# Optimization experiments

Measured on AMD Instinct MI355X. Metric: run time of the kernel, lower is better.

## Reference

```python
import jax, jax.numpy as jnp
import numpy as np

BATCH, SEQ_L, H, N = 16, 2048, 512, 64
DT_MIN, DT_MAX = 1e-3, 1e-1


def setup_inputs() -> dict:
    key = jax.random.key(0)
    ks = jax.random.split(key, 6)
    u = jax.random.normal(ks[0], (BATCH, SEQ_L, H), dtype=jnp.float32)
    # S4D diagonal init: stable real part, linearly spaced imaginary frequencies
    Lambda_real = -0.5 * jnp.ones((N,), dtype=jnp.float32)
    Lambda_imag = jnp.pi * jnp.arange(N, dtype=jnp.float32)
    B_real = jax.random.normal(ks[1], (H, N), dtype=jnp.float32) * (N ** -0.5)
    B_imag = jnp.zeros((H, N), dtype=jnp.float32)
    C_real = jax.random.normal(ks[2], (H, N), dtype=jnp.float32) * 0.5
    C_imag = jax.random.normal(ks[3], (H, N), dtype=jnp.float32) * 0.5
    log_dt = (jax.random.uniform(ks[4], (H,), dtype=jnp.float32)
              * (np.float32(np.log(DT_MAX)) - np.float32(np.log(DT_MIN)))
              + np.float32(np.log(DT_MIN)))
    D = jax.random.normal(ks[5], (H,), dtype=jnp.float32) * 0.01
    return {"u": u, "Lambda_real": Lambda_real, "Lambda_imag": Lambda_imag,
            "B_real": B_real, "B_imag": B_imag, "C_real": C_real,
            "C_imag": C_imag, "log_dt": log_dt, "D": D}


def reference(u, Lambda_real, Lambda_imag, B_real, B_imag, C_real, C_imag, log_dt, D):
    # u: (B, L, H)
    Lseq = u.shape[1]
    Lam = Lambda_real + 1j * Lambda_imag            # (N,)
    Bc = B_real + 1j * B_imag                        # (H, N)
    Cc = C_real + 1j * C_imag                        # (H, N)
    dt = jnp.exp(log_dt)                             # (H,)

    # ZOH discretization (matches step(): Ab = exp(dt*Lam), Bb = B*(Ab-1)/(Lam+eps))
    dtA = dt[:, None] * Lam[None, :]                 # (H, N)
    Ab = jnp.exp(dtA)
    Bb = Bc * (Ab - 1.0) / (Lam[None, :] + 1e-8)

    # Vandermonde over all channels at once: V[h,n,l] = exp(dt_h * Lam_n * l)
    ell = jnp.arange(Lseq, dtype=jnp.float32)
    V = jnp.exp(dtA[:, :, None] * ell[None, None, :])  # (H, N, L) complex
    K = jnp.einsum('hn,hnl->hl', Cc * Bb, V).real       # (H, L) real kernel

    # Causal FFT convolution along time
    x = jnp.swapaxes(u, -1, -2)                      # (B, H, L)
    nfft = 2 * Lseq
    Xf = jnp.fft.rfft(x, n=nfft)                     # (B, H, nfft/2+1)
    Kf = jnp.fft.rfft(K, n=nfft)                     # (H, nfft/2+1)
    y = jnp.fft.irfft(Xf * Kf[None], n=nfft)[..., :Lseq]

    y = y + x * D[None, :, None]                     # skip connection
    return jnp.swapaxes(y, -1, -2)                   # (B, L, H)
```

## Files before the change

### kernel.cpp

```cpp
#include <hip/hip_runtime.h>
#include <hip/hip_bf16.h>


#define BSZ 16
#define LSEQ 2048
#define HCH 512
#define NST 64
#define NF 4096

__device__ __forceinline__ int WD(int i) { return 2 * i + ((i >> 4) << 1); }

__device__ __forceinline__ float2 cadd(float2 a, float2 b) { return make_float2(a.x + b.x, a.y + b.y); }
__device__ __forceinline__ float2 csub(float2 a, float2 b) { return make_float2(a.x - b.x, a.y - b.y); }
__device__ __forceinline__ float2 cmul(float2 a, float c, float s) {
    return make_float2(a.x * c - a.y * s, a.x * s + a.y * c);
}
__device__ __forceinline__ float2 cmul2(float2 a, float2 b) {
    return make_float2(a.x * b.x - a.y * b.y, a.x * b.y + a.y * b.x);
}

__device__ __forceinline__ void sincos_red(float a, float* s, float* c) {
    double ad = (double)a;
    double q = rint(ad * 0.15915494309189535);
    float r = (float)(ad - q * 6.283185307179586);
    __sincosf(r, s, c);
}

template <bool INV>
__device__ __forceinline__ void dft8_tail(float2 t0, float2 t1, float2 t2, float2 t3,
                                          float2 t4, float2 t5, float2 t6, float2 t7,
                                          float2& A0, float2& A1, float2& A2, float2& A3,
                                          float2& A4, float2& A5, float2& A6, float2& A7)
{
    const float S = 0.70710678118654752f;
    float2 u0 = cadd(t0, t2), u2 = csub(t0, t2);
    float2 u1 = cadd(t1, t3), u3 = csub(t1, t3);
    A0 = cadd(u0, u1); A4 = csub(u0, u1);
    if constexpr (!INV) {
        A2 = make_float2(u2.x + u3.y, u2.y - u3.x);
        A6 = make_float2(u2.x - u3.y, u2.y + u3.x);
    } else {
        A2 = make_float2(u2.x - u3.y, u2.y + u3.x);
        A6 = make_float2(u2.x + u3.y, u2.y - u3.x);
    }
    float2 b0 = t4, b1, b2, b3;
    if constexpr (!INV) {
        b1 = make_float2(S * (t5.x + t5.y), S * (t5.y - t5.x));
        b2 = make_float2(t6.y, -t6.x);
        b3 = make_float2(S * (t7.y - t7.x), -S * (t7.x + t7.y));
    } else {
        b1 = make_float2(S * (t5.x - t5.y), S * (t5.y + t5.x));
        b2 = make_float2(-t6.y, t6.x);
        b3 = make_float2(-S * (t7.x + t7.y), S * (t7.x - t7.y));
    }
    float2 v0 = cadd(b0, b2), v2 = csub(b0, b2);
    float2 v1 = cadd(b1, b3), v3 = csub(b1, b3);
    A1 = cadd(v0, v1); A5 = csub(v0, v1);
    if constexpr (!INV) {
        A3 = make_float2(v2.x + v3.y, v2.y - v3.x);
        A7 = make_float2(v2.x - v3.y, v2.y + v3.x);
    } else {
        A3 = make_float2(v2.x - v3.y, v2.y + v3.x);
        A7 = make_float2(v2.x + v3.y, v2.y - v3.x);
    }
}

template <int SIDX, bool INV, bool HALF, int NT>
__device__ __forceinline__ void fft8_stage(float* z, int t)
{
    constexpr int lgQ = 9 - 3 * SIDX;
    constexpr int Q = 1 << lgQ;
    constexpr int ITERS = 512 / NT;
    const float asc = -1.5339807878856412e-3f * (float)(1 << (3 * SIDX));
#pragma unroll
    for (int it = 0; it < ITERS; ++it) {
        const int bb = t + NT * it;
        const int j = bb & (Q - 1);
        const int base = ((bb >> lgQ) << (lgQ + 3)) + j;
        float s1, c1;
        __sincosf(asc * (float)j, &s1, &c1);
        if constexpr (INV) s1 = -s1;
        const float c2 = c1 * c1 - s1 * s1, s2 = 2.f * c1 * s1;
        const float c3 = c1 * c2 - s1 * s2, s3 = c1 * s2 + s1 * c2;
        const float c4 = c2 * c2 - s2 * s2, s4 = 2.f * c2 * s2;
        const float c5 = c2 * c3 - s2 * s3, s5 = c2 * s3 + s2 * c3;
        const float c6 = c3 * c3 - s3 * s3, s6 = 2.f * c3 * s3;
        const float c7 = c3 * c4 - s3 * s4, s7 = c3 * s4 + s3 * c4;
        float2 a0 = *(float2*)&z[WD(base + 0 * Q)];
        float2 a1 = *(float2*)&z[WD(base + 1 * Q)];
        float2 a2 = *(float2*)&z[WD(base + 2 * Q)];
        float2 a3 = *(float2*)&z[WD(base + 3 * Q)];
        float2 a4, a5, a6, a7;
        if constexpr (!(HALF && !INV)) {
            a4 = *(float2*)&z[WD(base + 4 * Q)];
            a5 = *(float2*)&z[WD(base + 5 * Q)];
            a6 = *(float2*)&z[WD(base + 6 * Q)];
            a7 = *(float2*)&z[WD(base + 7 * Q)];
        }
        if constexpr (INV) {
            a1 = cmul(a1, c1, s1); a2 = cmul(a2, c2, s2); a3 = cmul(a3, c3, s3);
            a4 = cmul(a4, c4, s4); a5 = cmul(a5, c5, s5); a6 = cmul(a6, c6, s6);
            a7 = cmul(a7, c7, s7);
        }
        float2 t0, t1, t2, t3, t4, t5, t6, t7;
        if constexpr (HALF && !INV) {
            t0 = a0; t4 = a0; t1 = a1; t5 = a1; t2 = a2; t6 = a2; t3 = a3; t7 = a3;
        } else {
            t0 = cadd(a0, a4); t4 = csub(a0, a4);
            t1 = cadd(a1, a5); t5 = csub(a1, a5);
            t2 = cadd(a2, a6); t6 = csub(a2, a6);
            t3 = cadd(a3, a7); t7 = csub(a3, a7);
        }
        float2 A0, A1, A2, A3, A4, A5, A6, A7;
        dft8_tail<INV>(t0, t1, t2, t3, t4, t5, t6, t7, A0, A1, A2, A3, A4, A5, A6, A7);
        if constexpr (!INV) {
            A1 = cmul(A1, c1, s1); A2 = cmul(A2, c2, s2); A3 = cmul(A3, c3, s3);
            A4 = cmul(A4, c4, s4); A5 = cmul(A5, c5, s5); A6 = cmul(A6, c6, s6);
            A7 = cmul(A7, c7, s7);
        }
        *(float2*)&z[WD(base + 0 * Q)] = A0;
        *(float2*)&z[WD(base + 1 * Q)] = A1;
        *(float2*)&z[WD(base + 2 * Q)] = A2;
        *(float2*)&z[WD(base + 3 * Q)] = A3;
        if constexpr (!(HALF && INV)) {
            *(float2*)&z[WD(base + 4 * Q)] = A4;
            *(float2*)&z[WD(base + 5 * Q)] = A5;
            *(float2*)&z[WD(base + 6 * Q)] = A6;
            *(float2*)&z[WD(base + 7 * Q)] = A7;
        }
    }
}

template <int NT>
__device__ __forceinline__ void mid_stage(float* z, const float2* __restrict__ kf, int t)
{
    constexpr int ITERS = 512 / NT;
#pragma unroll
    for (int it = 0; it < ITERS; ++it) {
        const int bb = t + NT * it;
        const int base = bb * 8;
        float2 a[8];
#pragma unroll
        for (int r = 0; r < 8; ++r) a[r] = *(float2*)&z[WD(base + r)];
        float2 t0 = cadd(a[0], a[4]), t4 = csub(a[0], a[4]);
        float2 t1 = cadd(a[1], a[5]), t5 = csub(a[1], a[5]);
        float2 t2 = cadd(a[2], a[6]), t6 = csub(a[2], a[6]);
        float2 t3 = cadd(a[3], a[7]), t7 = csub(a[3], a[7]);
        float2 A0, A1, A2, A3, A4, A5, A6, A7;
        dft8_tail<false>(t0, t1, t2, t3, t4, t5, t6, t7, A0, A1, A2, A3, A4, A5, A6, A7);
        const float2* kp = kf + base;
        A0 = cmul2(A0, kp[0]); A1 = cmul2(A1, kp[1]);
        A2 = cmul2(A2, kp[2]); A3 = cmul2(A3, kp[3]);
        A4 = cmul2(A4, kp[4]); A5 = cmul2(A5, kp[5]);
        A6 = cmul2(A6, kp[6]); A7 = cmul2(A7, kp[7]);
        t0 = cadd(A0, A4); t4 = csub(A0, A4);
        t1 = cadd(A1, A5); t5 = csub(A1, A5);
        t2 = cadd(A2, A6); t6 = csub(A2, A6);
        t3 = cadd(A3, A7); t7 = csub(A3, A7);
        float2 X0, X1, X2, X3, X4, X5, X6, X7;
        dft8_tail<true>(t0, t1, t2, t3, t4, t5, t6, t7, X0, X1, X2, X3, X4, X5, X6, X7);
        *(float2*)&z[WD(base + 0)] = X0;
        *(float2*)&z[WD(base + 1)] = X1;
        *(float2*)&z[WD(base + 2)] = X2;
        *(float2*)&z[WD(base + 3)] = X3;
        *(float2*)&z[WD(base + 4)] = X4;
        *(float2*)&z[WD(base + 5)] = X5;
        *(float2*)&z[WD(base + 6)] = X6;
        *(float2*)&z[WD(base + 7)] = X7;
    }
}

__global__ __launch_bounds__(256) void k_kgen(const float* __restrict__ lam_r,
                                              const float* __restrict__ lam_i,
                                              const float* __restrict__ Br,
                                              const float* __restrict__ Bi,
                                              const float* __restrict__ Cr,
                                              const float* __restrict__ Ci,
                                              const float* __restrict__ log_dt,
                                              float* __restrict__ gKt)
{
    const int h = blockIdx.x >> 1;
    const int half = blockIdx.x & 1;
    const int t = threadIdx.x;
    __shared__ float sWr[NST], sWi[NST], sAr[NST], sAi[NST], sDr[NST], sDi[NST];

    if (t < NST) {
        const int n = t;
        float lr = lam_r[n], li = lam_i[n];
        float dt = __expf(log_dt[h]);
        float dar = dt * lr;
        float dai = dt * li;
        float e = __expf(dar);
        float sn, cs; sincos_red(dai, &sn, &cs);
        float Ar = e * cs, Ai = e * sn;
        float nr = Ar - 1.0f, ni = Ai;
        float br = Br[h * NST + n], bi = Bi[h * NST + n];
        float tr = br * nr - bi * ni;
        float ti = br * ni + bi * nr;
        float dr = lr + 1e-8f, di = li;
        float den = dr * dr + di * di;
        float bbr = (tr * dr + ti * di) / den;
        float bbi = (ti * dr - tr * di) / den;
        float cr = Cr[h * NST + n], ci = Ci[h * NST + n];
        sWr[n] = cr * bbr - ci * bbi;
        sWi[n] = cr * bbi + ci * bbr;
        sAr[n] = Ar; sAi[n] = Ai;
        sDr[n] = dar; sDi[n] = dai;
    }
    __syncthreads();

    const int l0 = half * 1024 + 4 * t;
    float acc[4] = {0.f, 0.f, 0.f, 0.f};
    const float fl0 = (float)l0;
    for (int n = 0; n < NST; ++n) {
        float dar = sDr[n], dai = sDi[n];
        float ang = dai * fl0;
        float sn, cs; sincos_red(ang, &sn, &cs);
        float e = __expf(dar * fl0);
        float pr = e * cs, pi = e * sn;
        float Ar = sAr[n], Ai = sAi[n];
        float wr = sWr[n], wi = sWi[n];
#pragma unroll
        for (int k = 0; k < 4; ++k) {
            acc[k] += wr * pr - wi * pi;
            float npr = pr * Ar - pi * Ai;
            pi = pr * Ai + pi * Ar;
            pr = npr;
        }
    }
    *(float4*)&gKt[(size_t)h * LSEQ + l0] = make_float4(acc[0], acc[1], acc[2], acc[3]);
}

__global__ __launch_bounds__(512) void k_fused(const float* __restrict__ gKt,
                                               float* __restrict__ gKf,
                                               const float* __restrict__ u,
                                               float* __restrict__ gut)
{
    const int bid = blockIdx.x;
    const int t = threadIdx.x;
    __shared__ float lds[8704];

    if (bid < HCH) {
        const int h = bid;
        float4 kv = ((const float4*)(gKt + (size_t)h * LSEQ))[t];
        int l = 4 * t;
        *(float2*)&lds[WD(l + 0)] = make_float2(kv.x, 0.f);
        *(float2*)&lds[WD(l + 1)] = make_float2(kv.y, 0.f);
        *(float2*)&lds[WD(l + 2)] = make_float2(kv.z, 0.f);
        *(float2*)&lds[WD(l + 3)] = make_float2(kv.w, 0.f);
        __syncthreads();
        fft8_stage<0, false, true , 512>(lds, t); __syncthreads();
        fft8_stage<1, false, false, 512>(lds, t); __syncthreads();
        fft8_stage<2, false, false, 512>(lds, t); __syncthreads();
        fft8_stage<3, false, false, 512>(lds, t); __syncthreads();
        float2* out = (float2*)gKf + (size_t)h * NF;
#pragma unroll
        for (int i = 0; i < 8; ++i) {
            int idx = t + 512 * i;
            out[idx] = *(float2*)&lds[WD(idx)];
        }
    } else {
        float (*tile)[65] = (float (*)[65])lds;
        const int tid2 = bid - HCH;
        const int b  = tid2 >> 8;
        const int ht = ((tid2 >> 5) & 7) * 64;
        const int lt = (tid2 & 31) * 64;
        const int tx = t & 15;
        const int ty = t >> 4;
        const float* inb = u + (size_t)b * LSEQ * HCH;
        float* outb = gut + (size_t)b * HCH * LSEQ;
#pragma unroll
        for (int i = 0; i < 2; ++i) {
            int r = ty + 32 * i;
            float4 v = *(const float4*)&inb[(size_t)(lt + r) * HCH + ht + 4 * tx];
            tile[r][4 * tx + 0] = v.x;
            tile[r][4 * tx + 1] = v.y;
            tile[r][4 * tx + 2] = v.z;
            tile[r][4 * tx + 3] = v.w;
        }
        __syncthreads();
#pragma unroll
        for (int i = 0; i < 2; ++i) {
            int rp = ty + 32 * i;
            float4 o = make_float4(tile[4 * tx + 0][rp], tile[4 * tx + 1][rp],
                                   tile[4 * tx + 2][rp], tile[4 * tx + 3][rp]);
            *(float4*)&outb[(size_t)(ht + rp) * LSEQ + lt + 4 * tx] = o;
        }
    }
}

__global__ __launch_bounds__(256) void k_transpose_bwd(const float* __restrict__ in,
                                                       float* __restrict__ out)
{
    __shared__ float tile[64][65];
    const int b  = blockIdx.z;
    const int lt = blockIdx.x * 64;
    const int ht = blockIdx.y * 64;
    const int tx = threadIdx.x;
    const int ty = threadIdx.y;
    const float* inb = in + (size_t)b * HCH * LSEQ;
    float* outb = out + (size_t)b * LSEQ * HCH;
#pragma unroll
    for (int i = 0; i < 4; ++i) {
        int r = ty + 16 * i;
        float4 v = *(const float4*)&inb[(size_t)(ht + r) * LSEQ + lt + 4 * tx];
        tile[r][4 * tx + 0] = v.x;
        tile[r][4 * tx + 1] = v.y;
        tile[r][4 * tx + 2] = v.z;
        tile[r][4 * tx + 3] = v.w;
    }
    __syncthreads();
#pragma unroll
    for (int i = 0; i < 4; ++i) {
        int rp = ty + 16 * i;
        float4 o = make_float4(tile[4 * tx + 0][rp], tile[4 * tx + 1][rp],
                               tile[4 * tx + 2][rp], tile[4 * tx + 3][rp]);
        *(float4*)&outb[(size_t)(lt + rp) * HCH + ht + 4 * tx] = o;
    }
}

__global__ __launch_bounds__(512, 4) void k_fftconv(float* __restrict__ gut,
                                                    const float* __restrict__ gKf,
                                                    const float* __restrict__ gD)
{
    const int bid = blockIdx.x;
    const int b = bid >> 9;
    const int h = bid & (HCH - 1);
    const int t = threadIdx.x;
    __shared__ float z[8704];

    float* row0 = gut + ((size_t)(b * HCH) + h) * LSEQ;
    float* row1 = gut + ((size_t)((b + 8) * HCH) + h) * LSEQ;

    float4 u0k = ((const float4*)row0)[t];
    float4 u1k = ((const float4*)row1)[t];
    {
        int l = 4 * t;
        *(float2*)&z[WD(l + 0)] = make_float2(u0k.x, u1k.x);
        *(float2*)&z[WD(l + 1)] = make_float2(u0k.y, u1k.y);
        *(float2*)&z[WD(l + 2)] = make_float2(u0k.z, u1k.z);
        *(float2*)&z[WD(l + 3)] = make_float2(u0k.w, u1k.w);
    }
    __syncthreads();

    fft8_stage<0, false, true , 512>(z, t); __syncthreads();
    fft8_stage<1, false, false, 512>(z, t); __syncthreads();
    fft8_stage<2, false, false, 512>(z, t); __syncthreads();
    mid_stage<512>(z, (const float2*)gKf + (size_t)h * NF, t); __syncthreads();
    fft8_stage<2, true, false, 512>(z, t); __syncthreads();
    fft8_stage<1, true, false, 512>(z, t); __syncthreads();
    fft8_stage<0, true, true , 512>(z, t); __syncthreads();

    const float sc = 1.0f / 4096.0f;
    const float Dh = gD[h];
    {
        int l = 4 * t;
        float2 z0 = *(float2*)&z[WD(l + 0)];
        float2 z1 = *(float2*)&z[WD(l + 1)];
        float2 z2 = *(float2*)&z[WD(l + 2)];
        float2 z3 = *(float2*)&z[WD(l + 3)];
        float4 o0 = make_float4(z0.x * sc + Dh * u0k.x, z1.x * sc + Dh * u0k.y,
                                z2.x * sc + Dh * u0k.z, z3.x * sc + Dh * u0k.w);
        float4 o1 = make_float4(z0.y * sc + Dh * u1k.x, z1.y * sc + Dh * u1k.y,
                                z2.y * sc + Dh * u1k.z, z3.y * sc + Dh * u1k.w);
        ((float4*)row0)[t] = o0;
        ((float4*)row1)[t] = o1;
    }
}

extern "C" void kernel_launch(void* const* d_in, const int* in_sizes, int n_in,
                              void* d_out, int out_size, void* d_ws, size_t ws_size,
                              hipStream_t stream)
{
    const float* u      = (const float*)d_in[0];
    const float* lam_r  = (const float*)d_in[1];
    const float* lam_i  = (const float*)d_in[2];
    const float* Br     = (const float*)d_in[3];
    const float* Bi     = (const float*)d_in[4];
    const float* Cr     = (const float*)d_in[5];
    const float* Ci     = (const float*)d_in[6];
    const float* log_dt = (const float*)d_in[7];
    const float* Dv     = (const float*)d_in[8];

    float* gut = (float*)d_ws;
    float* gKt = (float*)d_ws + (size_t)BSZ * HCH * LSEQ;
    float* gKf = (float*)d_out;

    k_kgen<<<2 * HCH, 256, 0, stream>>>(lam_r, lam_i, Br, Bi, Cr, Ci, log_dt, gKt);
    k_fused<<<HCH + 4096, 512, 0, stream>>>(gKt, gKf, u, gut);
    k_fftconv<<<BSZ / 2 * HCH, 512, 0, stream>>>(gut, gKf, Dv);
    k_transpose_bwd<<<dim3(LSEQ / 64, HCH / 64, BSZ), dim3(16, 16, 1), 0, stream>>>(gut, (float*)d_out);
}
```

Baseline: 231.8 us.

## Drop explicit transposes and read/write (B,L,H) layout directly in FFT conv

The FFT-convolution kernel now gathers u straight from the (B,L,H) input with strided per-element loads and scatters y straight into the output. This removes the forward and backward transpose passes and the intermediate workspace round trip. Kernel generation and the kernel's FFT are also fused into a single k_kfused kernel, so the time-domain kernel no longer goes through global memory. The cost is that the conv kernel's global accesses become uncoalesced, one 4-byte element per cache line at an HCH stride. Block ordering places neighbouring h channels close together so L2 can absorb some of that.

```diff
diff --git a/kernel.cpp b/kernel.cpp
--- a/kernel.cpp
+++ b/kernel.cpp
@@ -170,18 +170,18 @@
     }
 }
 
-__global__ __launch_bounds__(256) void k_kgen(const float* __restrict__ lam_r,
-                                              const float* __restrict__ lam_i,
-                                              const float* __restrict__ Br,
-                                              const float* __restrict__ Bi,
-                                              const float* __restrict__ Cr,
-                                              const float* __restrict__ Ci,
-                                              const float* __restrict__ log_dt,
-                                              float* __restrict__ gKt)
-{
-    const int h = blockIdx.x >> 1;
-    const int half = blockIdx.x & 1;
+__global__ __launch_bounds__(512) void k_kfused(const float* __restrict__ lam_r,
+                                                const float* __restrict__ lam_i,
+                                                const float* __restrict__ Br,
+                                                const float* __restrict__ Bi,
+                                                const float* __restrict__ Cr,
+                                                const float* __restrict__ Ci,
+                                                const float* __restrict__ log_dt,
+                                                float* __restrict__ gKf)
+{
+    const int h = blockIdx.x;
     const int t = threadIdx.x;
+    __shared__ float z[8704];
     __shared__ float sWr[NST], sWi[NST], sAr[NST], sAi[NST], sDr[NST], sDi[NST];
 
     if (t < NST) {
@@ -209,7 +209,7 @@
     }
     __syncthreads();
 
-    const int l0 = half * 1024 + 4 * t;
+    const int l0 = 4 * t;
     float acc[4] = {0.f, 0.f, 0.f, 0.f};
     const float fl0 = (float)l0;
     for (int n = 0; n < NST; ++n) {
@@ -228,119 +228,49 @@
             pr = npr;
         }
     }
-    *(float4*)&gKt[(size_t)h * LSEQ + l0] = make_float4(acc[0], acc[1], acc[2], acc[3]);
-}
-
-__global__ __launch_bounds__(512) void k_fused(const float* __restrict__ gKt,
-                                               float* __restrict__ gKf,
-                                               const float* __restrict__ u,
-                                               float* __restrict__ gut)
+    *(float2*)&z[WD(l0 + 0)] = make_float2(acc[0], 0.f);
+    *(float2*)&z[WD(l0 + 1)] = make_float2(acc[1], 0.f);
+    *(float2*)&z[WD(l0 + 2)] = make_float2(acc[2], 0.f);
+    *(float2*)&z[WD(l0 + 3)] = make_float2(acc[3], 0.f);
+    __syncthreads();
+
+    fft8_stage<0, false, true , 512>(z, t); __syncthreads();
+    fft8_stage<1, false, false, 512>(z, t); __syncthreads();
+    fft8_stage<2, false, false, 512>(z, t); __syncthreads();
+    fft8_stage<3, false, false, 512>(z, t); __syncthreads();
+
+    float2* outp = (float2*)gKf + (size_t)h * NF;
+#pragma unroll
+    for (int i = 0; i < 8; ++i) {
+        int idx = t + 512 * i;
+        outp[idx] = *(float2*)&z[WD(idx)];
+    }
+}
+
+__global__ __launch_bounds__(512, 4) void k_fftconv(const float* __restrict__ u,
+                                                    const float* __restrict__ gKf,
+                                                    const float* __restrict__ gD,
+                                                    float* __restrict__ y)
 {
     const int bid = blockIdx.x;
-    const int t = threadIdx.x;
-    __shared__ float lds[8704];
-
-    if (bid < HCH) {
-        const int h = bid;
-        float4 kv = ((const float4*)(gKt + (size_t)h * LSEQ))[t];
-        int l = 4 * t;
-        *(float2*)&lds[WD(l + 0)] = make_float2(kv.x, 0.f);
-        *(float2*)&lds[WD(l + 1)] = make_float2(kv.y, 0.f);
-        *(float2*)&lds[WD(l + 2)] = make_float2(kv.z, 0.f);
-        *(float2*)&lds[WD(l + 3)] = make_float2(kv.w, 0.f);
-        __syncthreads();
-        fft8_stage<0, false, true , 512>(lds, t); __syncthreads();
-        fft8_stage<1, false, false, 512>(lds, t); __syncthreads();
-        fft8_stage<2, false, false, 512>(lds, t); __syncthreads();
-        fft8_stage<3, false, false, 512>(lds, t); __syncthreads();
-        float2* out = (float2*)gKf + (size_t)h * NF;
-#pragma unroll
-        for (int i = 0; i < 8; ++i) {
-            int idx = t + 512 * i;
-            out[idx] = *(float2*)&lds[WD(idx)];
-        }
-    } else {
-        float (*tile)[65] = (float (*)[65])lds;
-        const int tid2 = bid - HCH;
-        const int b  = tid2 >> 8;
-        const int ht = ((tid2 >> 5) & 7) * 64;
-        const int lt = (tid2 & 31) * 64;
-        const int tx = t & 15;
-        const int ty = t >> 4;
-        const float* inb = u + (size_t)b * LSEQ * HCH;
-        float* outb = gut + (size_t)b * HCH * LSEQ;
-#pragma unroll
-        for (int i = 0; i < 2; ++i) {
-            int r = ty + 32 * i;
-            float4 v = *(const float4*)&inb[(size_t)(lt + r) * HCH + ht + 4 * tx];
-            tile[r][4 * tx + 0] = v.x;
-            tile[r][4 * tx + 1] = v.y;
-            tile[r][4 * tx + 2] = v.z;
-            tile[r][4 * tx + 3] = v.w;
-        }
-        __syncthreads();
-#pragma unroll
-        for (int i = 0; i < 2; ++i) {
-            int rp = ty + 32 * i;
-            float4 o = make_float4(tile[4 * tx + 0][rp], tile[4 * tx + 1][rp],
-                                   tile[4 * tx + 2][rp], tile[4 * tx + 3][rp]);
-            *(float4*)&outb[(size_t)(ht + rp) * LSEQ + lt + 4 * tx] = o;
-        }
-    }
-}
-
-__global__ __launch_bounds__(256) void k_transpose_bwd(const float* __restrict__ in,
-                                                       float* __restrict__ out)
-{
-    __shared__ float tile[64][65];
-    const int b  = blockIdx.z;
-    const int lt = blockIdx.x * 64;
-    const int ht = blockIdx.y * 64;
-    const int tx = threadIdx.x;
-    const int ty = threadIdx.y;
-    const float* inb = in + (size_t)b * HCH * LSEQ;
-    float* outb = out + (size_t)b * LSEQ * HCH;
-#pragma unroll
-    for (int i = 0; i < 4; ++i) {
-        int r = ty + 16 * i;
-        float4 v = *(const float4*)&inb[(size_t)(ht + r) * LSEQ + lt + 4 * tx];
-        tile[r][4 * tx + 0] = v.x;
-        tile[r][4 * tx + 1] = v.y;
-        tile[r][4 * tx + 2] = v.z;
-        tile[r][4 * tx + 3] = v.w;
-    }
-    __syncthreads();
-#pragma unroll
-    for (int i = 0; i < 4; ++i) {
-        int rp = ty + 16 * i;
-        float4 o = make_float4(tile[4 * tx + 0][rp], tile[4 * tx + 1][rp],
-                               tile[4 * tx + 2][rp], tile[4 * tx + 3][rp]);
-        *(float4*)&outb[(size_t)(lt + rp) * HCH + ht + 4 * tx] = o;
-    }
-}
-
-__global__ __launch_bounds__(512, 4) void k_fftconv(float* __restrict__ gut,
-                                                    const float* __restrict__ gKf,
-                                                    const float* __restrict__ gD)
-{
-    const int bid = blockIdx.x;
-    const int b = bid >> 9;
-    const int h = bid & (HCH - 1);
+    const int bp = bid & 7;
+    const int h  = bid >> 3;
     const int t = threadIdx.x;
     __shared__ float z[8704];
 
-    float* row0 = gut + ((size_t)(b * HCH) + h) * LSEQ;
-    float* row1 = gut + ((size_t)((b + 8) * HCH) + h) * LSEQ;
-
-    float4 u0k = ((const float4*)row0)[t];
-    float4 u1k = ((const float4*)row1)[t];
-    {
-        int l = 4 * t;
-        *(float2*)&z[WD(l + 0)] = make_float2(u0k.x, u1k.x);
-        *(float2*)&z[WD(l + 1)] = make_float2(u0k.y, u1k.y);
-        *(float2*)&z[WD(l + 2)] = make_float2(u0k.z, u1k.z);
-        *(float2*)&z[WD(l + 3)] = make_float2(u0k.w, u1k.w);
-    }
+    const size_t base0 = ((size_t)bp * LSEQ) * HCH + h;
+    const size_t base1 = ((size_t)(bp + 8) * LSEQ) * HCH + h;
+    const int l0 = 4 * t;
+
+    float u0k[4], u1k[4];
+#pragma unroll
+    for (int k = 0; k < 4; ++k) {
+        u0k[k] = u[base0 + (size_t)(l0 + k) * HCH];
+        u1k[k] = u[base1 + (size_t)(l0 + k) * HCH];
+    }
+#pragma unroll
+    for (int k = 0; k < 4; ++k)
+        *(float2*)&z[WD(l0 + k)] = make_float2(u0k[k], u1k[k]);
     __syncthreads();
 
     fft8_stage<0, false, true , 512>(z, t); __syncthreads();
@@ -353,18 +283,11 @@
 
     const float sc = 1.0f / 4096.0f;
     const float Dh = gD[h];
-    {
-        int l = 4 * t;
-        float2 z0 = *(float2*)&z[WD(l + 0)];
-        float2 z1 = *(float2*)&z[WD(l + 1)];
-        float2 z2 = *(float2*)&z[WD(l + 2)];
-        float2 z3 = *(float2*)&z[WD(l + 3)];
-        float4 o0 = make_float4(z0.x * sc + Dh * u0k.x, z1.x * sc + Dh * u0k.y,
-                                z2.x * sc + Dh * u0k.z, z3.x * sc + Dh * u0k.w);
-        float4 o1 = make_float4(z0.y * sc + Dh * u1k.x, z1.y * sc + Dh * u1k.y,
-                                z2.y * sc + Dh * u1k.z, z3.y * sc + Dh * u1k.w);
-        ((float4*)row0)[t] = o0;
-        ((float4*)row1)[t] = o1;
+#pragma unroll
+    for (int k = 0; k < 4; ++k) {
+        float2 zz = *(float2*)&z[WD(l0 + k)];
+        y[base0 + (size_t)(l0 + k) * HCH] = zz.x * sc + Dh * u0k[k];
+        y[base1 + (size_t)(l0 + k) * HCH] = zz.y * sc + Dh * u1k[k];
     }
 }
 
@@ -382,12 +305,8 @@
     const float* log_dt = (const float*)d_in[7];
     const float* Dv     = (const float*)d_in[8];
 
-    float* gut = (float*)d_ws;
-    float* gKt = (float*)d_ws + (size_t)BSZ * HCH * LSEQ;
-    float* gKf = (float*)d_out;
-
-    k_kgen<<<2 * HCH, 256, 0, stream>>>(lam_r, lam_i, Br, Bi, Cr, Ci, log_dt, gKt);
-    k_fused<<<HCH + 4096, 512, 0, stream>>>(gKt, gKf, u, gut);
-    k_fftconv<<<BSZ / 2 * HCH, 512, 0, stream>>>(gut, gKf, Dv);
-    k_transpose_bwd<<<dim3(LSEQ / 64, HCH / 64, BSZ), dim3(16, 16, 1), 0, stream>>>(gut, (float*)d_out);
-}
+    float* gKf = (float*)d_ws;
+
+    k_kfused<<<HCH, 512, 0, stream>>>(lam_r, lam_i, Br, Bi, Cr, Ci, log_dt, gKf);
+    k_fftconv<<<BSZ / 2 * HCH, 512, 0, stream>>>(u, gKf, Dv, (float*)d_out);
+}
```

After: 294.1 us. 1.27x slower.
